# Kernel optimization log

Measured on AMD Instinct MI355X. Metric: run time of the kernel, lower is better.

## Reference

```python
import jax, jax.numpy as jnp
import numpy as np


def mish(x):
    return x * jnp.tanh(jax.nn.softplus(x))


def gcn(x, W, b, src, dst):
    # PyG GCNConv: h = D^-1/2 (A+I) D^-1/2 (x W) + b, aggregation at dst=edge_index[1]
    n = x.shape[0]
    h = x @ W
    deg = jax.ops.segment_sum(jnp.ones(src.shape[0], x.dtype), dst, num_segments=n) + 1.0
    dinv = jax.lax.rsqrt(deg)
    msg = h[src] * (dinv[src] * dinv[dst])[:, None]
    agg = jax.ops.segment_sum(msg, dst, num_segments=n)
    return agg + h * (dinv * dinv)[:, None] + b


def pool_mean(x, seg, num_segments):
    s = jax.ops.segment_sum(x, seg, num_segments=num_segments)
    c = jax.ops.segment_sum(jnp.ones(x.shape[0], x.dtype), seg, num_segments=num_segments)
    return s / jnp.maximum(c, 1.0)[:, None]


def attention(x, qW, qb, kW, kb, vW, vb, G):
    # x: [G*R, in_feats] -> per-graph self-attention over ROIs (dropout is identity in eval)
    R = x.shape[0] // G
    xc = x.reshape(G, R, x.shape[1])
    Q = xc @ qW + qb
    K = xc @ kW + kb
    Vv = xc @ vW + vb
    scores = jnp.einsum('gqd,gkd->gqk', Q, K) / (Q.shape[-1] ** 0.5)
    w = jax.nn.softmax(scores, axis=-1)
    out = jnp.einsum('gqk,gkd->gqd', w, Vv).reshape(G * R, Vv.shape[-1])
    return out, w.mean(axis=0)


def closs(a, b, temp=0.6):
    a = a / jnp.maximum(jnp.linalg.norm(a, axis=1, keepdims=True), 1e-12)
    b = b / jnp.maximum(jnp.linalg.norm(b, axis=1, keepdims=True), 1e-12)
    logits = (a @ b.T) / temp
    return -jnp.mean(jnp.diagonal(jax.nn.log_softmax(logits, axis=1)))


def setup_inputs() -> dict:
    key = jax.random.key(0)
    G, R1, R2, F_IN, H, OUT, DEG, V = 512, 200, 160, 128, 64, 64, 16, 64
    N1, N2 = G * R1, G * R2
    ks = iter(jax.random.split(key, 64))
    d = {}
    d['x1'] = jax.random.normal(next(ks), (N1, R1 + 3), jnp.float32)
    d['x2'] = jax.random.normal(next(ks), (N2, R2 + 3), jnp.float32)

    def lin(name, i, o):
        d[name + '_W'] = jax.random.normal(next(ks), (i, o), jnp.float32) * (i ** -0.5)
        d[name + '_b'] = jnp.zeros((o,), jnp.float32)

    lin('fcl', R1 + 3, F_IN); lin('fcr', R2 + 3, F_IN)
    lin('fcl1', R1, F_IN); lin('fcr1', R2, F_IN)
    lin('a1_q', F_IN, OUT); lin('a1_k', F_IN, OUT); lin('a1_v', F_IN, OUT)
    lin('a2_q', F_IN, OUT); lin('a2_k', F_IN, OUT); lin('a2_v', F_IN, OUT)
    lin('conv', F_IN, H); lin('conv1', H, H)
    lin('mlp', H, OUT)
    lin('fc1a', OUT * 4, F_IN); lin('fc1b', F_IN, 2)

    def edges(k, R):
        k1, k2 = jax.random.split(k)
        off = (jnp.arange(G, dtype=jnp.int32) * R)[:, None]
        src = jax.random.randint(k1, (G, R * DEG), 0, R, jnp.int32) + off
        dst = jax.random.randint(k2, (G, R * DEG), 0, R, jnp.int32) + off
        return jnp.stack([src.reshape(-1), dst.reshape(-1)])

    d['edge_index1'] = edges(next(ks), R1)
    d['edge_index2'] = edges(next(ks), R2)
    d['batch1'] = jnp.repeat(jnp.arange(G, dtype=jnp.int32), R1)
    d['batch2'] = jnp.repeat(jnp.arange(G, dtype=jnp.int32), R2)

    def sub(k, R):
        # one visited-node set (as in RW_subgraph) tiled per graph with offsets
        vis = jnp.sort(jax.random.permutation(k, R)[:V]).astype(jnp.int32)
        return (vis[None, :] + (jnp.arange(G, dtype=jnp.int32) * R)[:, None]).reshape(-1)

    d['sub_idx1'] = sub(next(ks), R1)
    d['sub_idx2'] = sub(next(ks), R2)
    d['num_graphs'] = G
    return d


def reference(x1, x2, fcl_W, fcl_b, fcr_W, fcr_b, fcl1_W, fcl1_b, fcr1_W, fcr1_b,
              a1_q_W, a1_q_b, a1_k_W, a1_k_b, a1_v_W, a1_v_b,
              a2_q_W, a2_q_b, a2_k_W, a2_k_b, a2_v_W, a2_v_b,
              conv_W, conv_b, conv1_W, conv1_b, mlp_W, mlp_b,
              fc1a_W, fc1a_b, fc1b_W, fc1b_b,
              edge_index1, edge_index2, batch1, batch2, sub_idx1, sub_idx2, num_graphs):
    G = int(num_graphs)
    src1, dst1 = edge_index1[0], edge_index1[1]
    src2, dst2 = edge_index2[0], edge_index2[1]

    z1 = x1[:, :-3] @ fcl1_W + fcl1_b
    z2 = x2[:, :-3] @ fcr1_W + fcr1_b
    z1, aw1 = attention(z1, a1_q_W, a1_q_b, a1_k_W, a1_k_b, a1_v_W, a1_v_b, G)
    z2, aw2 = attention(z2, a2_q_W, a2_q_b, a2_k_W, a2_k_b, a2_v_W, a2_v_b, G)
    z1 = pool_mean(z1, batch1, G)
    z2 = pool_mean(z2, batch2, G)

    h1 = x1 @ fcl_W + fcl_b
    h2 = x2 @ fcr_W + fcr_b
    o1 = mish(gcn(h1, conv_W, conv_b, src1, dst1))
    o2 = mish(gcn(h2, conv_W, conv_b, src2, dst2))
    o1 = gcn(o1, conv1_W, conv1_b, src1, dst1)
    o2 = gcn(o2, conv1_W, conv1_b, src2, dst2)

    s1 = o1[sub_idx1] @ mlp_W + mlp_b
    s2 = o2[sub_idx2] @ mlp_W + mlp_b
    s1 = pool_mean(s1, batch1[sub_idx1], G)
    s2 = pool_mean(s2, batch2[sub_idx2], G)

    c_loss = closs(s1, z2) + closs(z1, s2)
    feat = jnp.concatenate([s1, z1, s2, z2], axis=1)
    out = mish(feat @ fc1a_W + fc1a_b) @ fc1b_W + fc1b_b
    return c_loss, out, aw1, aw2
```

## Files before the change

kernel.cpp:

```cpp
#include <hip/hip_runtime.h>
#include <math.h>

#define TPB 256
#define MAXR 200
#define MAXE 3200

typedef float f32x4 __attribute__((ext_vector_type(4)));
typedef __bf16 bfv8 __attribute__((ext_vector_type(8)));

union U8 { uint4 q; unsigned short us[8]; __bf16 b[8]; bfv8 v; };

__device__ __forceinline__ unsigned short f2bfu(float f) {
  union { __bf16 h; unsigned short u; } x;
  x.h = (__bf16)f;
  return x.u;
}
__device__ __forceinline__ float bfu2f(unsigned short u) {
  return __uint_as_float((unsigned)u << 16);
}

__device__ __forceinline__ float mish_f(float x) {
  float sp = fmaxf(x, 0.f) + log1pf(expf(-fabsf(x)));
  return x * tanhf(sp);
}

__device__ __forceinline__ U8 loadA_f32(const float* Af, int kb, int K, bool rowok) {
  U8 u;
  if (rowok && kb + 8 <= K) {
    float4 f0 = *(const float4*)(Af + kb);
    float4 f1 = *(const float4*)(Af + kb + 4);
    u.b[0]=(__bf16)f0.x; u.b[1]=(__bf16)f0.y; u.b[2]=(__bf16)f0.z; u.b[3]=(__bf16)f0.w;
    u.b[4]=(__bf16)f1.x; u.b[5]=(__bf16)f1.y; u.b[6]=(__bf16)f1.z; u.b[7]=(__bf16)f1.w;
  } else {
#pragma unroll
    for (int j = 0; j < 8; ++j) {
      float f = (rowok && kb + j < K) ? Af[kb + j] : 0.f;
      u.b[j] = (__bf16)f;
    }
  }
  return u;
}

template<bool ABF16, bool CBF16, int NJ, int KPMAX>
__global__ __launch_bounds__(256) void gemm2(
    const void* __restrict__ Av, const unsigned short* __restrict__ Bt,
    const float* __restrict__ bias, void* __restrict__ Cv,
    int N, int M, int K, int lda, int ldc,
    long sA, long sB, long sC, float alpha, int Kpad)
{
  constexpr int BM = NJ * 16;
  __shared__ unsigned short Bs[BM * KPMAX];

  const int tid = threadIdx.x;
  const int col0 = blockIdx.x * BM, row0 = blockIdx.y * 64;

  {
    const unsigned short* Bp = Bt + (long)blockIdx.z * sB + (long)col0 * Kpad;
    int rows = M - col0; if (rows > BM) rows = BM;
    const int total = rows * Kpad;
    for (int i = tid * 8; i < total; i += TPB * 32) {
      uint4 a0, a1, a2, a3;
      bool b1 = i + TPB * 8  < total;
      bool b2 = i + TPB * 16 < total;
      bool b3 = i + TPB * 24 < total;
      a0 = *(const uint4*)&Bp[i];
      if (b1) a1 = *(const uint4*)&Bp[i + TPB * 8];
      if (b2) a2 = *(const uint4*)&Bp[i + TPB * 16];
      if (b3) a3 = *(const uint4*)&Bp[i + TPB * 24];
      *(uint4*)&Bs[i] = a0;
      if (b1) *(uint4*)&Bs[i + TPB * 8]  = a1;
      if (b2) *(uint4*)&Bs[i + TPB * 16] = a2;
      if (b3) *(uint4*)&Bs[i + TPB * 24] = a3;
    }
  }

  const int lane = tid & 63, w = tid >> 6;
  const int mrow = lane & 15, kg = lane >> 4;
  const int arow = row0 + w * 16 + mrow;
  const bool rowok = arow < N;

  const unsigned short* Ah = nullptr;
  const float* Af = nullptr;
  if (ABF16) Ah = (const unsigned short*)Av + (long)blockIdx.z * sA + (long)arow * lda;
  else       Af = (const float*)Av + (long)blockIdx.z * sA + (long)arow * lda;

  U8 ua;
  if (ABF16) ua.q = *(const uint4*)(Ah + kg * 8);
  else       ua   = loadA_f32(Af, kg * 8, K, rowok);

  __syncthreads();

  f32x4 acc[NJ];
#pragma unroll
  for (int j = 0; j < NJ; ++j) acc[j] = (f32x4)0.f;

  for (int k0 = 0; k0 < K; k0 += 32) {
    U8 un;
    bool more = (k0 + 32) < K;
    if (more) {
      if (ABF16) un.q = *(const uint4*)(Ah + k0 + 32 + kg * 8);
      else       un   = loadA_f32(Af, k0 + 32 + kg * 8, K, rowok);
    }
    const int kb = k0 + kg * 8;
#pragma unroll
    for (int j = 0; j < NJ; ++j) {
      U8 ub;
      ub.q = *(const uint4*)&Bs[(j * 16 + mrow) * Kpad + kb];
      acc[j] = __builtin_amdgcn_mfma_f32_16x16x32_bf16(ua.v, ub.v, acc[j], 0, 0, 0);
    }
    if (more) ua = un;
  }

  long cbase = (long)blockIdx.z * sC;
#pragma unroll
  for (int j = 0; j < NJ; ++j) {
    int gc = col0 + j * 16 + mrow;
    if (gc >= M) continue;
    float bb = bias ? bias[gc] : 0.f;
#pragma unroll
    for (int r = 0; r < 4; ++r) {
      int gr = row0 + w * 16 + kg * 4 + r;
      if (gr >= N) continue;
      float v = acc[j][r] * alpha + bb;
      if (CBF16) ((unsigned short*)Cv)[cbase + (long)gr * ldc + gc] = f2bfu(v);
      else       ((float*)Cv)[cbase + (long)gr * ldc + gc] = v;
    }
  }
}

static inline int kpad_of(int K) { return ((K + 31) / 32) * 32 + 8; }

struct PrepSeg { const float* src; void* dst; int K, M, Kpad, kind; };
struct PrepArgs { PrepSeg s[19]; };

__global__ __launch_bounds__(256) void prep_weights(PrepArgs a) {
  PrepSeg sg = a.s[blockIdx.x];
  if (sg.kind == 0) {
    unsigned short* d = (unsigned short*)sg.dst;
    int tot = sg.M * sg.Kpad;
    for (int i = threadIdx.x; i < tot; i += TPB) {
      int m = i / sg.Kpad, k = i - m * sg.Kpad;
      float f = (k < sg.K) ? sg.src[(long)k * sg.M + m] : 0.f;
      d[i] = f2bfu(f);
    }
  } else {
    float* d = (float*)sg.dst;
    for (int i = threadIdx.x; i < sg.K; i += TPB) d[i] = sg.src[i];
  }
}

__global__ __launch_bounds__(256) void xcast(const float* __restrict__ x,
                                             unsigned short* __restrict__ xb,
                                             int C, int S)
{
  long r0 = (long)blockIdx.x * 8;
  for (int i = threadIdx.x; i < 8 * S; i += TPB) {
    int rr = i / S, c = i - rr * S;
    long r = r0 + rr;
    xb[r * S + c] = f2bfu(c < C ? x[r * C + c] : 0.f);
  }
}

__global__ __launch_bounds__(256) void ktvt_kernel(
    const unsigned short* __restrict__ QKV, unsigned short* __restrict__ Kt,
    unsigned short* __restrict__ Vt, int R, int Rpad)
{
  int g = blockIdx.x;
  const unsigned short* q = QKV + (long)g * R * 192;
  unsigned short* kt = Kt + (long)g * R * 72;
  unsigned short* vt = Vt + (long)g * 64 * Rpad;
  int c = threadIdx.x & 63, w = threadIdx.x >> 6;
  for (int r = w; r < R; r += 4) {
    kt[r * 72 + c] = q[(long)r * 192 + 64 + c];
    vt[c * Rpad + r] = q[(long)r * 192 + 128 + c];
  }
  int pad = Rpad - R;
  for (int i = threadIdx.x; i < 64 * pad; i += TPB) {
    int cc = i / pad, k = i - cc * pad;
    vt[cc * Rpad + R + k] = 0;
  }
}

__global__ __launch_bounds__(256) void gcn_kernel(
    const unsigned short* __restrict__ hWb, const int* __restrict__ src,
    const int* __restrict__ dst, const float* __restrict__ bias,
    unsigned short* __restrict__ outb, int R, int EPG, int do_mish)
{
  __shared__ float hWs[MAXR * 64];
  __shared__ float dinv_s[MAXR];
  __shared__ unsigned short ssrc[MAXE];
  __shared__ int cnt[256];
  __shared__ int scan[256];
  __shared__ int offx[257];
  __shared__ int cur[256];

  int g = blockIdx.x, tid = threadIdx.x;
  long base = (long)g * R * 64;
  long ebase = (long)g * EPG;
  int gR = g * R;
  int RF = R * 64;

  cnt[tid] = 0;
  __syncthreads();
  for (int e = tid; e < EPG; e += TPB)
    atomicAdd(&cnt[dst[ebase + e] - gR], 1);
  __syncthreads();

  int x = cnt[tid];
  scan[tid] = x;
  __syncthreads();
#pragma unroll
  for (int s = 1; s < 256; s <<= 1) {
    int t = (tid >= s) ? scan[tid - s] : 0;
    __syncthreads();
    scan[tid] += t;
    __syncthreads();
  }
  if (tid == 0) offx[0] = 0;
  offx[tid + 1] = scan[tid];
  cur[tid] = scan[tid] - x;
  if (tid < R) dinv_s[tid] = rsqrtf((float)cnt[tid] + 1.f);
  __syncthreads();

  for (int e = tid; e < EPG; e += TPB) {
    int d = dst[ebase + e] - gR;
    int s = src[ebase + e] - gR;
    int pos = atomicAdd(&cur[d], 1);
    ssrc[pos] = (unsigned short)s;
  }
  for (int i = tid * 8; i < RF; i += TPB * 8) {
    U8 u; u.q = *(const uint4*)&hWb[base + i];
    float4 f0, f1;
    f0.x = bfu2f(u.us[0]); f0.y = bfu2f(u.us[1]); f0.z = bfu2f(u.us[2]); f0.w = bfu2f(u.us[3]);
    f1.x = bfu2f(u.us[4]); f1.y = bfu2f(u.us[5]); f1.z = bfu2f(u.us[6]); f1.w = bfu2f(u.us[7]);
    *(float4*)&hWs[i] = f0;
    *(float4*)&hWs[i + 4] = f1;
  }
  __syncthreads();

  int lane = tid & 63, w = tid >> 6;
  for (int d = w; d < R; d += 4) {
    int i = offx[d], eEnd = offx[d + 1];
    float acc = 0.f;
    for (; i + 4 <= eEnd; i += 4) {
      int s0 = ssrc[i], s1 = ssrc[i + 1], s2 = ssrc[i + 2], s3 = ssrc[i + 3];
      float p0 = dinv_s[s0] * hWs[(s0 << 6) | lane];
      float p1 = dinv_s[s1] * hWs[(s1 << 6) | lane];
      float p2 = dinv_s[s2] * hWs[(s2 << 6) | lane];
      float p3 = dinv_s[s3] * hWs[(s3 << 6) | lane];
      acc += p0 + p1 + p2 + p3;
    }
    for (; i < eEnd; ++i) {
      int s = ssrc[i];
      acc += dinv_s[s] * hWs[(s << 6) | lane];
    }
    float di = dinv_s[d];
    float v = di * acc + hWs[(d << 6) | lane] * di * di + bias[lane];
    if (do_mish) v = mish_f(v);
    outb[base + ((long)d << 6) + lane] = f2bfu(v);
  }
}

__global__ __launch_bounds__(256) void softmax_bf16(unsigned short* __restrict__ S,
                                                    int R, long rows)
{
  long wid = (long)blockIdx.x * 4 + (threadIdx.x >> 6);
  if (wid >= rows) return;
  int lane = threadIdx.x & 63;
  unsigned short* row = S + wid * R;
  float v[4];
  float mx = -1e30f;
#pragma unroll
  for (int t = 0; t < 4; ++t) {
    int j = lane + t * 64;
    v[t] = (j < R) ? bfu2f(row[j]) : -1e30f;
    mx = fmaxf(mx, v[t]);
  }
#pragma unroll
  for (int o = 32; o; o >>= 1) mx = fmaxf(mx, __shfl_xor(mx, o));
  float s = 0.f;
#pragma unroll
  for (int t = 0; t < 4; ++t) {
    int j = lane + t * 64;
    if (j < R) { v[t] = expf(v[t] - mx); s += v[t]; }
  }
#pragma unroll
  for (int o = 32; o; o >>= 1) s += __shfl_xor(s, o);
  float inv = 1.f / s;
#pragma unroll
  for (int t = 0; t < 4; ++t) {
    int j = lane + t * 64;
    if (j < R) row[j] = f2bfu(v[t] * inv);
  }
}

__global__ void meang_bf16(const unsigned short* __restrict__ S, float* __restrict__ out,
                           int RR, int G, float inv)
{
  int idx = blockIdx.x * TPB + threadIdx.x;
  if (idx >= RR) return;
  const unsigned short* p = S + idx;
  float s = 0.f;
  for (int g = 0; g + 8 <= G; g += 8) {
    s += bfu2f(p[(long)g * RR])       + bfu2f(p[(long)(g + 1) * RR]) +
         bfu2f(p[(long)(g + 2) * RR]) + bfu2f(p[(long)(g + 3) * RR]) +
         bfu2f(p[(long)(g + 4) * RR]) + bfu2f(p[(long)(g + 5) * RR]) +
         bfu2f(p[(long)(g + 6) * RR]) + bfu2f(p[(long)(g + 7) * RR]);
  }
  out[idx] = s * inv;
}

__global__ __launch_bounds__(64) void pool_mean_kernel(const float* __restrict__ X,
                                                       float* __restrict__ out, int R)
{
  int g = blockIdx.x, lane = threadIdx.x;
  const float* p = X + (long)g * R * 64 + lane;
  float s = 0.f;
  for (int r = 0; r + 4 <= R; r += 4)
    s += p[(long)r * 64] + p[(long)(r + 1) * 64] + p[(long)(r + 2) * 64] + p[(long)(r + 3) * 64];
  out[g * 64 + lane] = s * (1.f / R);
}

__global__ __launch_bounds__(64) void sub_mean_kernel(const unsigned short* __restrict__ X,
                                                      const int* __restrict__ sub,
                                                      float* __restrict__ out, int V)
{
  int g = blockIdx.x, lane = threadIdx.x;
  float s = 0.f;
  for (int v = 0; v + 4 <= V; v += 4) {
    int i0 = sub[g * V + v],     i1 = sub[g * V + v + 1];
    int i2 = sub[g * V + v + 2], i3 = sub[g * V + v + 3];
    s += bfu2f(X[(long)i0 * 64 + lane]) + bfu2f(X[(long)i1 * 64 + lane]) +
         bfu2f(X[(long)i2 * 64 + lane]) + bfu2f(X[(long)i3 * 64 + lane]);
  }
  out[g * 64 + lane] = s * (1.f / V);
}

__global__ __launch_bounds__(64) void norm_rows_kernel(const float* __restrict__ X,
                                                       float* __restrict__ Y)
{
  int g = blockIdx.x, lane = threadIdx.x;
  float x = X[g * 64 + lane];
  float ss = x * x;
#pragma unroll
  for (int o = 32; o; o >>= 1) ss += __shfl_xor(ss, o);
  float n = fmaxf(sqrtf(ss), 1e-12f);
  Y[g * 64 + lane] = x / n;
}

__global__ __launch_bounds__(256) void closs_kernel(const float* __restrict__ An,
                                                    const float* __restrict__ Bn,
                                                    float* __restrict__ loss, int G,
                                                    float invTemp, float coef)
{
  int i = blockIdx.x;
  __shared__ float arow[64];
  __shared__ float logits[512];
  __shared__ float red[256];
  int t = threadIdx.x;
  if (t < 64) arow[t] = An[i * 64 + t];
  __syncthreads();
  for (int j = t; j < G; j += 256) {
    const float* bp = Bn + (long)j * 64;
    float d = 0.f;
#pragma unroll
    for (int k = 0; k < 64; ++k) d = fmaf(arow[k], bp[k], d);
    logits[j] = d * invTemp;
  }
  __syncthreads();
  float mx = -1e30f;
  for (int j = t; j < G; j += 256) mx = fmaxf(mx, logits[j]);
  red[t] = mx; __syncthreads();
  for (int o = 128; o; o >>= 1) { if (t < o) red[t] = fmaxf(red[t], red[t + o]); __syncthreads(); }
  mx = red[0]; __syncthreads();
  float s = 0.f;
  for (int j = t; j < G; j += 256) s += expf(logits[j] - mx);
  red[t] = s; __syncthreads();
  for (int o = 128; o; o >>= 1) { if (t < o) red[t] += red[t + o]; __syncthreads(); }
  if (t == 0) {
    float lse = mx + logf(red[0]);
    atomicAdd(loss, coef * (lse - logits[i]));
  }
}

__global__ __launch_bounds__(128) void head_kernel(
    const float* __restrict__ s1, const float* __restrict__ z1,
    const float* __restrict__ s2, const float* __restrict__ z2,
    const float* __restrict__ W1, const float* __restrict__ b1,
    const float* __restrict__ W2, const float* __restrict__ b2,
    float* __restrict__ out)
{
  int g = blockIdx.x, t = threadIdx.x;
  __shared__ float feat[256];
  __shared__ float hid[128];
  if (t < 64) {
    feat[t]       = s1[g * 64 + t];
    feat[64 + t]  = z1[g * 64 + t];
    feat[128 + t] = s2[g * 64 + t];
    feat[192 + t] = z2[g * 64 + t];
  }
  __syncthreads();
  float acc = b1[t];
  for (int k = 0; k < 256; ++k) acc = fmaf(feat[k], W1[k * 128 + t], acc);
  hid[t] = mish_f(acc);
  __syncthreads();
  if (t < 2) {
    float a2 = b2[t];
#pragma unroll
    for (int k = 0; k < 128; ++k) a2 = fmaf(hid[k], W2[k * 2 + t], a2);
    out[g * 2 + t] = a2;
  }
}

#define LAUNCH_GEMM(ABF,CBF,NJ,KP, A,B,BI,C, N,M,K,LDA,LDC,SA,SB,SC,BAT,AL,KPAD) \
  { dim3 g_(((M)+(NJ)*16-1)/((NJ)*16), ((N)+63)/64, (BAT)); \
    gemm2<ABF,CBF,NJ,KP><<<g_,256,0,stream>>>((A),(B),(BI),(C),(N),(M),(K),(LDA),(LDC),(SA),(SB),(SC),(AL),(KPAD)); }

extern "C" void kernel_launch(void* const* d_in, const int* in_sizes, int n_in,
                              void* d_out, int out_size, void* d_ws, size_t ws_size,
                              hipStream_t stream)
{
  const float* x1     = (const float*)d_in[0];
  const float* x2     = (const float*)d_in[1];
  const float* fcl_W  = (const float*)d_in[2];  const float* fcl_b  = (const float*)d_in[3];
  const float* fcr_W  = (const float*)d_in[4];  const float* fcr_b  = (const float*)d_in[5];
  const float* fcl1_W = (const float*)d_in[6];  const float* fcl1_b = (const float*)d_in[7];
  const float* fcr1_W = (const float*)d_in[8];  const float* fcr1_b = (const float*)d_in[9];
  const float* a1qW = (const float*)d_in[10]; const float* a1qb = (const float*)d_in[11];
  const float* a1kW = (const float*)d_in[12]; const float* a1kb = (const float*)d_in[13];
  const float* a1vW = (const float*)d_in[14]; const float* a1vb = (const float*)d_in[15];
  const float* a2qW = (const float*)d_in[16]; const float* a2qb = (const float*)d_in[17];
  const float* a2kW = (const float*)d_in[18]; const float* a2kb = (const float*)d_in[19];
  const float* a2vW = (const float*)d_in[20]; const float* a2vb = (const float*)d_in[21];
  const float* convW  = (const float*)d_in[22]; const float* convb  = (const float*)d_in[23];
  const float* conv1W = (const float*)d_in[24]; const float* conv1b = (const float*)d_in[25];
  const float* mlpW   = (const float*)d_in[26]; const float* mlpb   = (const float*)d_in[27];
  const float* fc1aW  = (const float*)d_in[28]; const float* fc1ab  = (const float*)d_in[29];
  const float* fc1bW  = (const float*)d_in[30]; const float* fc1bb  = (const float*)d_in[31];
  const int* ei1  = (const int*)d_in[32];
  const int* ei2  = (const int*)d_in[33];
  const int* sub1 = (const int*)d_in[36];
  const int* sub2 = (const int*)d_in[37];

  const int R1 = in_sizes[6] / 128;
  const int R2 = in_sizes[8] / 128;
  const int N1 = in_sizes[34];
  const int N2 = in_sizes[35];
  const int G  = N1 / R1;
  const int E1 = in_sizes[32] / 2, E2 = in_sizes[33] / 2;
  const int EPG1 = E1 / G, EPG2 = E2 / G;
  const int V = in_sizes[36] / G;

  const int XS = 232;
  const int Kp1  = kpad_of(R1);
  const int Kp2  = kpad_of(R2);
  const int Kp1f = kpad_of(R1 + 3);
  const int Kp2f = kpad_of(R2 + 3);
  const int Rpad1 = Kp1, Rpad2 = Kp2;

  char* wp = (char*)d_ws;
  auto alloc = [&](size_t bytes) -> char* {
    char* p = wp; wp += (bytes + 255) & ~(size_t)255; return p;
  };
  unsigned short* x1b = (unsigned short*)alloc((size_t)N1 * XS * 2);
  unsigned short* x2b = (unsigned short*)alloc((size_t)N2 * XS * 2);
  size_t raSh = (size_t)G * R1 * R1;
  if ((size_t)N1 * 128 > raSh) raSh = (size_t)N1 * 128;
  unsigned short* RA = (unsigned short*)alloc(raSh * 2);
  unsigned short* RB = (unsigned short*)alloc((size_t)N1 * 192 * 2);
  unsigned short* Kt = (unsigned short*)alloc((size_t)G * R1 * 72 * 2);
  unsigned short* Vt = (unsigned short*)alloc((size_t)G * 64 * Rpad1 * 2);
  float* W5 = (float*)alloc((size_t)N1 * 64 * 4);
  unsigned short* fcl1t  = (unsigned short*)alloc((size_t)128 * Kp1 * 2);
  unsigned short* fcr1t  = (unsigned short*)alloc((size_t)128 * Kp2 * 2);
  unsigned short* fclt   = (unsigned short*)alloc((size_t)128 * Kp1f * 2);
  unsigned short* fcrt   = (unsigned short*)alloc((size_t)128 * Kp2f * 2);
  unsigned short* Wc1t   = (unsigned short*)alloc((size_t)192 * 136 * 2);
  unsigned short* Wc2t   = (unsigned short*)alloc((size_t)192 * 136 * 2);
  unsigned short* convt  = (unsigned short*)alloc((size_t)64 * 136 * 2);
  unsigned short* conv1t = (unsigned short*)alloc((size_t)64 * 72 * 2);
  unsigned short* mlpt   = (unsigned short*)alloc((size_t)64 * 72 * 2);
  float* bc1 = (float*)alloc(192 * 4);
  float* bc2 = (float*)alloc(192 * 4);
  float* Pz1 = (float*)alloc((size_t)G * 64 * 4);
  float* Pz2 = (float*)alloc((size_t)G * 64 * 4);
  float* Ps1 = (float*)alloc((size_t)G * 64 * 4);
  float* Ps2 = (float*)alloc((size_t)G * 64 * 4);
  float* Mt  = (float*)alloc((size_t)G * 64 * 4);
  float* n_s1 = (float*)alloc((size_t)G * 64 * 4);
  float* n_z2 = (float*)alloc((size_t)G * 64 * 4);
  float* n_z1 = (float*)alloc((size_t)G * 64 * 4);
  float* n_s2 = (float*)alloc((size_t)G * 64 * 4);
  (void)alloc(4096);

  float* loss = (float*)d_out;
  float* outp = loss + 1;
  float* aw1  = outp + (size_t)G * 2;
  float* aw2  = aw1 + (size_t)R1 * R1;

  hipMemsetAsync(d_out, 0, sizeof(float), stream);

  PrepArgs pa;
  int seg = 0;
  auto addp = [&](const float* s, unsigned short* d, int K, int M, int Kp) {
    pa.s[seg].src = s; pa.s[seg].dst = d; pa.s[seg].K = K; pa.s[seg].M = M;
    pa.s[seg].Kpad = Kp; pa.s[seg].kind = 0; seg++;
  };
  auto addb = [&](const float* s, float* d, int n) {
    pa.s[seg].src = s; pa.s[seg].dst = d; pa.s[seg].K = n; pa.s[seg].M = 0;
    pa.s[seg].Kpad = 0; pa.s[seg].kind = 1; seg++;
  };
  addp(fcl1_W, fcl1t, R1, 128, Kp1);
  addp(fcr1_W, fcr1t, R2, 128, Kp2);
  addp(fcl_W,  fclt,  R1 + 3, 128, Kp1f);
  addp(fcr_W,  fcrt,  R2 + 3, 128, Kp2f);
  addp(a1qW, Wc1t,             128, 64, 136);
  addp(a1kW, Wc1t + 64 * 136,  128, 64, 136);
  addp(a1vW, Wc1t + 128 * 136, 128, 64, 136);
  addp(a2qW, Wc2t,             128, 64, 136);
  addp(a2kW, Wc2t + 64 * 136,  128, 64, 136);
  addp(a2vW, Wc2t + 128 * 136, 128, 64, 136);
  addp(convW,  convt,  128, 64, 136);
  addp(conv1W, conv1t, 64, 64, 72);
  addp(mlpW,   mlpt,   64, 64, 72);
  addb(a1qb, bc1, 64); addb(a1kb, bc1 + 64, 64); addb(a1vb, bc1 + 128, 64);
  addb(a2qb, bc2, 64); addb(a2kb, bc2 + 64, 64); addb(a2vb, bc2 + 128, 64);
  prep_weights<<<seg, 256, 0, stream>>>(pa);

  xcast<<<N1 / 8, 256, 0, stream>>>(x1, x1b, R1 + 3, XS);
  xcast<<<N2 / 8, 256, 0, stream>>>(x2, x2b, R2 + 3, XS);

  LAUNCH_GEMM(true, true, 8, 232, x1b, fcl1t, fcl1_b, RA,
              N1, 128, R1, XS, 128, 0, 0, 0, 1, 1.f, Kp1);
  LAUNCH_GEMM(true, true, 12, 136, RA, Wc1t, bc1, RB,
              N1, 192, 128, 128, 192, 0, 0, 0, 1, 1.f, 136);
  ktvt_kernel<<<G, 256, 0, stream>>>(RB, Kt, Vt, R1, Rpad1);
  LAUNCH_GEMM(true, true, 8, 72, RB, Kt, nullptr, RA,
              R1, R1, 64, 192, R1, (long)R1 * 192, (long)R1 * 72, (long)R1 * R1,
              G, 0.125f, 72);
  {
    long rows = (long)G * R1;
    softmax_bf16<<<(int)((rows + 3) / 4), 256, 0, stream>>>(RA, R1, rows);
    meang_bf16<<<(R1 * R1 + TPB - 1) / TPB, TPB, 0, stream>>>(RA, aw1, R1 * R1, G, 1.f / G);
  }
  LAUNCH_GEMM(true, false, 4, 232, RA, Vt, nullptr, W5,
              R1, 64, R1, R1, 64, (long)R1 * R1, (long)64 * Rpad1, (long)R1 * 64,
              G, 1.f, Rpad1);
  pool_mean_kernel<<<G, 64, 0, stream>>>(W5, Pz1, R1);

  LAUNCH_GEMM(true, true, 8, 232, x2b, fcr1t, fcr1_b, RA,
              N2, 128, R2, XS, 128, 0, 0, 0, 1, 1.f, Kp2);
  LAUNCH_GEMM(true, true, 12, 136, RA, Wc2t, bc2, RB,
              N2, 192, 128, 128, 192, 0, 0, 0, 1, 1.f, 136);
  ktvt_kernel<<<G, 256, 0, stream>>>(RB, Kt, Vt, R2, Rpad2);
  LAUNCH_GEMM(true, true, 8, 72, RB, Kt, nullptr, RA,
              R2, R2, 64, 192, R2, (long)R2 * 192, (long)R2 * 72, (long)R2 * R2,
              G, 0.125f, 72);
  {
    long rows = (long)G * R2;
    softmax_bf16<<<(int)((rows + 3) / 4), 256, 0, stream>>>(RA, R2, rows);
    meang_bf16<<<(R2 * R2 + TPB - 1) / TPB, TPB, 0, stream>>>(RA, aw2, R2 * R2, G, 1.f / G);
  }
  LAUNCH_GEMM(true, false, 4, 232, RA, Vt, nullptr, W5,
              R2, 64, R2, R2, 64, (long)R2 * R2, (long)64 * Rpad2, (long)R2 * 64,
              G, 1.f, Rpad2);
  pool_mean_kernel<<<G, 64, 0, stream>>>(W5, Pz2, R2);

  unsigned short* hW0 = RB;
  unsigned short* hW1 = RB + (size_t)N1 * 64;
  unsigned short* hW2 = RB + (size_t)N1 * 128;
  LAUNCH_GEMM(true, true, 8, 232, x1b, fclt, fcl_b, RA,
              N1, 128, R1 + 3, XS, 128, 0, 0, 0, 1, 1.f, Kp1f);
  LAUNCH_GEMM(true, true, 4, 136, RA, convt, nullptr, hW0,
              N1, 64, 128, 128, 64, 0, 0, 0, 1, 1.f, 136);
  gcn_kernel<<<G, 256, 0, stream>>>(hW0, ei1, ei1 + E1, convb, hW1, R1, EPG1, 1);
  LAUNCH_GEMM(true, true, 4, 136, hW1, conv1t, nullptr, hW2,
              N1, 64, 64, 64, 64, 0, 0, 0, 1, 1.f, 72);
  gcn_kernel<<<G, 256, 0, stream>>>(hW2, ei1, ei1 + E1, conv1b, hW0, R1, EPG1, 0);
  sub_mean_kernel<<<G, 64, 0, stream>>>(hW0, sub1, Mt, V);
  LAUNCH_GEMM(false, false, 4, 136, Mt, mlpt, mlpb, Ps1,
              G, 64, 64, 64, 64, 0, 0, 0, 1, 1.f, 72);

  LAUNCH_GEMM(true, true, 8, 232, x2b, fcrt, fcr_b, RA,
              N2, 128, R2 + 3, XS, 128, 0, 0, 0, 1, 1.f, Kp2f);
  LAUNCH_GEMM(true, true, 4, 136, RA, convt, nullptr, hW0,
              N2, 64, 128, 128, 64, 0, 0, 0, 1, 1.f, 136);
  gcn_kernel<<<G, 256, 0, stream>>>(hW0, ei2, ei2 + E2, convb, hW1, R2, EPG2, 1);
  LAUNCH_GEMM(true, true, 4, 136, hW1, conv1t, nullptr, hW2,
              N2, 64, 64, 64, 64, 0, 0, 0, 1, 1.f, 72);
  gcn_kernel<<<G, 256, 0, stream>>>(hW2, ei2, ei2 + E2, conv1b, hW0, R2, EPG2, 0);
  sub_mean_kernel<<<G, 64, 0, stream>>>(hW0, sub2, Mt, V);
  LAUNCH_GEMM(false, false, 4, 136, Mt, mlpt, mlpb, Ps2,
              G, 64, 64, 64, 64, 0, 0, 0, 1, 1.f, 72);

  norm_rows_kernel<<<G, 64, 0, stream>>>(Ps1, n_s1);
  norm_rows_kernel<<<G, 64, 0, stream>>>(Pz2, n_z2);
  norm_rows_kernel<<<G, 64, 0, stream>>>(Pz1, n_z1);
  norm_rows_kernel<<<G, 64, 0, stream>>>(Ps2, n_s2);
  const float invTemp = 1.f / 0.6f;
  closs_kernel<<<G, 256, 0, stream>>>(n_s1, n_z2, loss, G, invTemp, 1.f / G);
  closs_kernel<<<G, 256, 0, stream>>>(n_z1, n_s2, loss, G, invTemp, 1.f / G);

  head_kernel<<<G, 128, 0, stream>>>(Ps1, Pz1, Ps2, Pz2, fc1aW, fc1ab, fc1bW, fc1bb, outp);
}
```

Measured before the change: 1.031 ms.

## Store pre-scaled bf16 features in LDS and pad edge lists to 8

The GCN aggregation kernel now keeps node features in shared memory as bf16 already multiplied by the source node's dinv, which halves the LDS footprint and removes a per-edge multiply. Each destination's edge list is padded to a multiple of 8 with a dummy index that points at a zeroed row, so the inner loop can read 8 source indices in one 16-byte load with no remainder loop. In exchange there is extra padding work, a fill pass over the ssrc buffer, and an additional bf16 rounding of the scaled features, which lowers precision slightly.

```diff
diff --git a/kernel.cpp b/kernel.cpp
--- a/kernel.cpp
+++ b/kernel.cpp
@@ -3,7 +3,7 @@
 
 #define TPB 256
 #define MAXR 200
-#define MAXE 3200
+#define MAXEP 4608
 
 typedef float f32x4 __attribute__((ext_vector_type(4)));
 typedef __bf16 bfv8 __attribute__((ext_vector_type(8)));
@@ -186,9 +186,9 @@
     const int* __restrict__ dst, const float* __restrict__ bias,
     unsigned short* __restrict__ outb, int R, int EPG, int do_mish)
 {
-  __shared__ float hWs[MAXR * 64];
+  __shared__ unsigned short hWs[(MAXR + 1) * 64];
   __shared__ float dinv_s[MAXR];
-  __shared__ unsigned short ssrc[MAXE];
+  __shared__ unsigned short ssrc[MAXEP];
   __shared__ int cnt[256];
   __shared__ int scan[256];
   __shared__ int offx[257];
@@ -207,7 +207,8 @@
   __syncthreads();
 
   int x = cnt[tid];
-  scan[tid] = x;
+  int pc = (x + 7) & ~7;
+  scan[tid] = pc;
   __syncthreads();
 #pragma unroll
   for (int s = 1; s < 256; s <<= 1) {
@@ -218,8 +219,12 @@
   }
   if (tid == 0) offx[0] = 0;
   offx[tid + 1] = scan[tid];
-  cur[tid] = scan[tid] - x;
-  if (tid < R) dinv_s[tid] = rsqrtf((float)cnt[tid] + 1.f);
+  cur[tid] = scan[tid] - pc;
+  if (tid < R) dinv_s[tid] = rsqrtf((float)x + 1.f);
+  {
+    unsigned dummy2 = (unsigned)R | ((unsigned)R << 16);
+    for (int i = tid; i < MAXEP / 2; i += TPB) ((unsigned*)ssrc)[i] = dummy2;
+  }
   __syncthreads();
 
   for (int e = tid; e < EPG; e += TPB) {
@@ -230,32 +235,32 @@
   }
   for (int i = tid * 8; i < RF; i += TPB * 8) {
     U8 u; u.q = *(const uint4*)&hWb[base + i];
-    float4 f0, f1;
-    f0.x = bfu2f(u.us[0]); f0.y = bfu2f(u.us[1]); f0.z = bfu2f(u.us[2]); f0.w = bfu2f(u.us[3]);
-    f1.x = bfu2f(u.us[4]); f1.y = bfu2f(u.us[5]); f1.z = bfu2f(u.us[6]); f1.w = bfu2f(u.us[7]);
-    *(float4*)&hWs[i] = f0;
-    *(float4*)&hWs[i + 4] = f1;
-  }
+    float di = dinv_s[i >> 6];
+#pragma unroll
+    for (int j = 0; j < 8; ++j) u.us[j] = f2bfu(bfu2f(u.us[j]) * di);
+    *(uint4*)&hWs[i] = u.q;
+  }
+  if (tid < 64) hWs[(R << 6) | tid] = 0;
   __syncthreads();
 
   int lane = tid & 63, w = tid >> 6;
   for (int d = w; d < R; d += 4) {
     int i = offx[d], eEnd = offx[d + 1];
     float acc = 0.f;
-    for (; i + 4 <= eEnd; i += 4) {
-      int s0 = ssrc[i], s1 = ssrc[i + 1], s2 = ssrc[i + 2], s3 = ssrc[i + 3];
-      float p0 = dinv_s[s0] * hWs[(s0 << 6) | lane];
-      float p1 = dinv_s[s1] * hWs[(s1 << 6) | lane];
-      float p2 = dinv_s[s2] * hWs[(s2 << 6) | lane];
-      float p3 = dinv_s[s3] * hWs[(s3 << 6) | lane];
-      acc += p0 + p1 + p2 + p3;
-    }
-    for (; i < eEnd; ++i) {
-      int s = ssrc[i];
-      acc += dinv_s[s] * hWs[(s << 6) | lane];
+    for (; i < eEnd; i += 8) {
+      U8 u; u.q = *(const uint4*)&ssrc[i];
+      float a0 = bfu2f(hWs[((int)u.us[0] << 6) | lane]);
+      float a1 = bfu2f(hWs[((int)u.us[1] << 6) | lane]);
+      float a2 = bfu2f(hWs[((int)u.us[2] << 6) | lane]);
+      float a3 = bfu2f(hWs[((int)u.us[3] << 6) | lane]);
+      float a4 = bfu2f(hWs[((int)u.us[4] << 6) | lane]);
+      float a5 = bfu2f(hWs[((int)u.us[5] << 6) | lane]);
+      float a6 = bfu2f(hWs[((int)u.us[6] << 6) | lane]);
+      float a7 = bfu2f(hWs[((int)u.us[7] << 6) | lane]);
+      acc += ((a0 + a1) + (a2 + a3)) + ((a4 + a5) + (a6 + a7));
     }
     float di = dinv_s[d];
-    float v = di * acc + hWs[(d << 6) | lane] * di * di + bias[lane];
+    float v = di * (acc + bfu2f(hWs[(d << 6) | lane])) + bias[lane];
     if (do_mish) v = mish_f(v);
     outb[base + ((long)d << 6) + lane] = f2bfu(v);
   }
```

Measured after the change: 941.5 us. 8.7% less time.
